# Kernel optimization log

Hardware: AMD Instinct MI355X
Metric: run time of the kernel (lower is better)

Reference implementation:

```python
import jax, jax.numpy as jnp
import numpy as np
from math import pi

FC_IN, FC_OUT = 64, 64
LABEL_NC = 35
B, C, H, W = 2, 64, 128, 128
EPS = 1e-5
SLOPE = 0.01  # torch leaky_relu default


def _pa(h, w):
    # absolute normalized coordinates, matches init_pos buffers
    xs = (jnp.arange(h, dtype=jnp.float32) / h) * 2.0 - 1.0
    ys = (jnp.arange(w, dtype=jnp.float32) / w) * 2.0 - 1.0
    px = jnp.broadcast_to(xs[:, None], (h, w))
    py = jnp.broadcast_to(ys[None, :], (h, w))
    return jnp.stack([px, py], 0)  # (2,h,w)


def _coords(h, w):
    # f0=3; while-loop runs once (f=3 -> f=1), so exactly 4 channels
    f = 3.0
    ang_x = 2.0 * pi * jnp.remainder(jnp.arange(w, dtype=jnp.float32), f) / f
    ang_y = 2.0 * pi * jnp.remainder(jnp.arange(h, dtype=jnp.float32), f) / f
    xcos = jnp.broadcast_to(jnp.cos(ang_x)[None, :], (h, w))
    xsin = jnp.broadcast_to(jnp.sin(ang_x)[None, :], (h, w))
    ycos = jnp.broadcast_to(jnp.cos(ang_y)[:, None], (h, w))
    ysin = jnp.broadcast_to(jnp.sin(ang_y)[:, None], (h, w))
    return jnp.stack([xcos, xsin, ycos, ysin], 0)  # (4,h,w)


def _nearest(t, h, w):
    # F.interpolate(mode='nearest') index map: floor(i*in/out)
    ih = jnp.arange(h) * t.shape[2] // h
    iw = jnp.arange(w) * t.shape[3] // w
    return t[:, :, ih][:, :, :, iw]


def setup_inputs() -> dict:
    key = jax.random.key(0)
    ks = jax.random.split(key, 7)
    return {
        "x": jax.random.normal(ks[0], (B, C, H, W), jnp.float32),
        "layout": jax.random.normal(ks[1], (B, LABEL_NC, H, W), jnp.float32),
        "pr": jax.random.normal(ks[2], (B, 2, H, W), jnp.float32),
        "conv_w": jax.random.normal(ks[3], (1, 10), jnp.float32) * 0.02,
        "conv_b": jnp.zeros((1,), jnp.float32),
        "W_table": jax.random.normal(ks[4], (LABEL_NC, FC_IN * FC_OUT), jnp.float32),
        "b_table": jax.random.normal(ks[5], (LABEL_NC, FC_OUT), jnp.float32) * 0.02,
        "pl": jax.random.normal(ks[6], (2, H, W), jnp.float32),
    }


def reference(x, layout, pr, conv_w, conv_b, W_table, b_table, pl):
    b, c, h, w = x.shape
    pa = jnp.broadcast_to(_pa(h, w)[None], (b, 2, h, w))
    plb = jnp.broadcast_to(pl[None], (b, 2, h, w))
    coords = jnp.broadcast_to(_coords(h, w)[None], (b, 4, h, w))
    prr = _nearest(pr, h, w)
    pos = jnp.concatenate([pa, plb, prr, coords], axis=1)  # (B,10,h,w)
    # 1x1 conv to a single channel, broadcast-added over C
    x = x + jnp.einsum('bchw,oc->bohw', pos, conv_w) + conv_b[None, :, None, None]
    # argmax-routed per-pixel affine params
    lay = _nearest(layout, h, w)
    arg = jnp.argmax(lay, axis=1)  # (B,h,w) int
    Wg = W_table[arg].reshape(b, h, w, FC_IN, FC_OUT)  # huge gathered tensor (as in original)
    bg = b_table[arg]  # (B,h,w,FC_OUT)
    xh = jnp.transpose(x, (0, 2, 3, 1))  # (B,h,w,C)
    y = jnp.einsum('bhwc,bhwco->bhwo', xh, Wg) + bg
    y = jnp.transpose(y, (0, 3, 1, 2))  # (B,FC_OUT,h,w)
    # instance norm (no affine, biased variance, eps=1e-5)
    mu = jnp.mean(y, axis=(2, 3), keepdims=True)
    var = jnp.var(y, axis=(2, 3), keepdims=True)
    y = (y - mu) * jax.lax.rsqrt(var + EPS)
    return jnp.where(y >= 0, y, SLOPE * y)
```

## Files before the change

kernel.cpp:

```cpp
#include <hip/hip_runtime.h>

#define HH 128
#define WW 128
#define NPIX (HH*WW)
#define NC 35
#define NB1 512
#define NCHK 16
#define CAP (NCHK*64)
#define NGB (NC*NCHK)
#define NG (2*NGB)

__global__ __launch_bounds__(256) void prep_kernel(
    const float* __restrict__ x, const float* __restrict__ layout,
    const float* __restrict__ pr, const float* __restrict__ cw,
    const float* __restrict__ cb, const float* __restrict__ pl,
    float* __restrict__ xt, int* __restrict__ argbuf, int* __restrict__ hist)
{
    __shared__ float s_t[64*65];
    __shared__ float s_s[64];
    __shared__ int   s_hist[NC];

    const int t  = threadIdx.x;
    const int bk = blockIdx.x;
    const int b  = bk >> 8;
    const int p0 = (bk & 255) << 6;
    const int h  = p0 >> 7;
    const int w0 = p0 & 127;

    if (t < NC) s_hist[t] = 0;

    const float4* x4 = (const float4*)x + (size_t)b*64*4096 + (p0 >> 2);
    #pragma unroll
    for (int k = 0; k < 4; ++k) {
        int f = k*256 + t;
        int c = f >> 4, i = f & 15;
        float4 q = x4[c*4096 + i];
        int base = c*65 + i*4;
        s_t[base+0]=q.x; s_t[base+1]=q.y; s_t[base+2]=q.z; s_t[base+3]=q.w;
    }

    int bi = -1;
    if (t < 64) {
        int w = w0 + t;
        float pxv = (float)h * (2.0f/128.0f) - 1.0f;
        float pyv = (float)w * (2.0f/128.0f) - 1.0f;
        float pl0 = pl[h*WW + w];
        float pl1 = pl[NPIX + h*WW + w];
        float pr0 = pr[((b*2+0)*HH + h)*WW + w];
        float pr1 = pr[((b*2+1)*HH + h)*WW + w];
        int kx = w % 3, kyy = h % 3;
        const float C1 = -0.5f, S1 = 0.86602540378443864676f;
        float xcv = (kx==0)  ? 1.0f : C1;
        float xsv = (kx==0)  ? 0.0f : ((kx==1)  ? S1 : -S1);
        float ycv = (kyy==0) ? 1.0f : C1;
        float ysv = (kyy==0) ? 0.0f : ((kyy==1) ? S1 : -S1);
        s_s[t] = cb[0] + pxv*cw[0] + pyv*cw[1] + pl0*cw[2] + pl1*cw[3]
               + pr0*cw[4] + pr1*cw[5] + xcv*cw[6] + xsv*cw[7]
               + ycv*cw[8] + ysv*cw[9];
    } else if (t < 128) {
        int lane = t - 64;
        const float* lp = layout + (size_t)(b*NC)*NPIX + p0 + lane;
        float best = lp[0]; int bj = 0;
        #pragma unroll
        for (int c = 1; c < NC; ++c) {
            float v = lp[(size_t)c*NPIX];
            if (v > best) { best = v; bj = c; }
        }
        bi = bj;
        argbuf[b*NPIX + p0 + lane] = bj;
    }
    __syncthreads();

    if (bi >= 0) atomicAdd(&s_hist[bi], 1);

    float4* xt4 = (float4*)xt + ((size_t)b*NPIX + p0)*16;
    #pragma unroll
    for (int k = 0; k < 4; ++k) {
        int g = k*256 + t;
        int p = g >> 4, c4 = g & 15;
        float sp = s_s[p];
        float4 q;
        q.x = s_t[(c4*4+0)*65 + p] + sp;
        q.y = s_t[(c4*4+1)*65 + p] + sp;
        q.z = s_t[(c4*4+2)*65 + p] + sp;
        q.w = s_t[(c4*4+3)*65 + p] + sp;
        xt4[p*16 + c4] = q;
    }
    __syncthreads();
    if (t < NC) hist[t*NB1 + bk] = s_hist[t];
}

__global__ __launch_bounds__(256) void scan_kernel(
    const int* __restrict__ hist, int* __restrict__ boff, int* __restrict__ cnt)
{
    __shared__ int s[256];
    const int e = blockIdx.x;
    const int b = e / NC, l = e % NC;
    const int t = threadIdx.x;
    int v = hist[l*NB1 + b*256 + t];
    s[t] = v;
    __syncthreads();
    #pragma unroll
    for (int off = 1; off < 256; off <<= 1) {
        int nv = (t >= off) ? s[t-off] : 0;
        __syncthreads();
        s[t] += nv;
        __syncthreads();
    }
    boff[l*NB1 + b*256 + t] = s[t] - v;
    if (t == 255) cnt[e] = s[255];
}

__global__ __launch_bounds__(64) void scatter_kernel(
    const int* __restrict__ argbuf, const int* __restrict__ boff,
    int* __restrict__ list)
{
    __shared__ int s_loc[NC];
    const int t  = threadIdx.x;
    const int bk = blockIdx.x;
    const int b  = bk >> 8;
    const int p0 = (bk & 255) << 6;
    if (t < NC) s_loc[t] = 0;
    __syncthreads();
    int l = argbuf[b*NPIX + p0 + t];
    int r = atomicAdd(&s_loc[l], 1);
    int pos = boff[l*NB1 + bk] + r;
    list[(b*NC + l)*CAP + pos] = p0 + t;
}

__global__ __launch_bounds__(256) void gemm_kernel(
    const float* __restrict__ Wt, const float* __restrict__ bt,
    const float* __restrict__ xt, const int* __restrict__ cnt,
    const int* __restrict__ list, float* __restrict__ yt,
    float* __restrict__ psum, float* __restrict__ pss)
{
    const int g     = blockIdx.x;
    const int bl    = g >> 4;
    const int chunk = g & (NCHK-1);
    const int t = threadIdx.x, wv = t >> 6, lane = t & 63;
    const int n = cnt[bl];
    const int base = chunk * 64;
    if (base >= n) {
        if (wv == 0) { psum[lane*NG + g] = 0.f; pss[lane*NG + g] = 0.f; }
        return;
    }
    const int m = min(64, n - base);
    const int b = bl / NC, l = bl % NC;

    __shared__ float s_x[64*64];
    __shared__ int   s_pix[64];
    __shared__ float s_red[4][64][2];

    if (t < 64) s_pix[t] = (t < m) ? list[bl*CAP + base + t] : 0;
    __syncthreads();

    {
        int p = t >> 2, j = t & 3;
        if (p < m) {
            const float4* r = (const float4*)xt + ((size_t)b*NPIX + s_pix[p])*16;
            #pragma unroll
            for (int k = 0; k < 4; ++k)
                ((float4*)(s_x + p*64 + j*16))[k] = r[j*4 + k];
        }
    }

    float Wcol[64];
    const float* Wl = Wt + l*4096 + lane;
    #pragma unroll
    for (int c = 0; c < 64; ++c) Wcol[c] = Wl[c*64];
    float bias = bt[l*64 + lane];
    __syncthreads();

    float ssum = 0.f, sss = 0.f;
    for (int i = 0; i < 16; ++i) {
        int p = wv*16 + i;
        if (p < m) {
            float acc = bias;
            const float4* xr = (const float4*)(s_x + p*64);
            #pragma unroll
            for (int c4 = 0; c4 < 16; ++c4) {
                float4 xq = xr[c4];
                acc = fmaf(xq.x, Wcol[4*c4+0], acc);
                acc = fmaf(xq.y, Wcol[4*c4+1], acc);
                acc = fmaf(xq.z, Wcol[4*c4+2], acc);
                acc = fmaf(xq.w, Wcol[4*c4+3], acc);
            }
            yt[((size_t)b*NPIX + s_pix[p])*64 + lane] = acc;
            ssum += acc; sss += acc*acc;
        }
    }
    s_red[wv][lane][0] = ssum;
    s_red[wv][lane][1] = sss;
    __syncthreads();
    if (wv == 0) {
        float S  = s_red[0][lane][0]+s_red[1][lane][0]+s_red[2][lane][0]+s_red[3][lane][0];
        float SS = s_red[0][lane][1]+s_red[1][lane][1]+s_red[2][lane][1]+s_red[3][lane][1];
        psum[lane*NG + g] = S;
        pss [lane*NG + g] = SS;
    }
}

__global__ __launch_bounds__(256) void stats_kernel(
    const float* __restrict__ psum, const float* __restrict__ pss,
    float* __restrict__ stats)
{
    __shared__ float red[256][2];
    const int e = blockIdx.x;
    const int b = e >> 6, o = e & 63;
    const int t = threadIdx.x;
    float S = 0.f, SS = 0.f;
    for (int gl = t; gl < NGB; gl += 256) {
        int g = b*NGB + gl;
        S  += psum[o*NG + g];
        SS += pss [o*NG + g];
    }
    red[t][0] = S; red[t][1] = SS;
    __syncthreads();
    #pragma unroll
    for (int s = 128; s > 0; s >>= 1) {
        if (t < s) { red[t][0] += red[t+s][0]; red[t][1] += red[t+s][1]; }
        __syncthreads();
    }
    if (t == 0) {
        const float invN = 1.0f/16384.0f;
        float mean = red[0][0] * invN;
        float var  = red[0][1] * invN - mean*mean;
        stats[e*2+0] = mean;
        stats[e*2+1] = rsqrtf(var + 1e-5f);
    }
}

__global__ __launch_bounds__(256) void norm_kernel(
    const float* __restrict__ yt, const float* __restrict__ stats,
    float* __restrict__ out)
{
    __shared__ float s_t[64*65];
    __shared__ float s_mean[64], s_rstd[64];

    const int t  = threadIdx.x;
    const int bk = blockIdx.x;
    const int b  = bk >> 8;
    const int p0 = (bk & 255) << 6;

    if (t < 64) {
        s_mean[t] = stats[(b*64+t)*2+0];
        s_rstd[t] = stats[(b*64+t)*2+1];
    }

    const float4* y4 = (const float4*)yt + ((size_t)b*NPIX + p0)*16;
    #pragma unroll
    for (int k = 0; k < 4; ++k) {
        int g = k*256 + t;
        int p = g >> 4, o4 = g & 15;
        float4 q = y4[p*16 + o4];
        int base = (o4*4)*65 + p;
        s_t[base]     = q.x;
        s_t[base+65]  = q.y;
        s_t[base+130] = q.z;
        s_t[base+195] = q.w;
    }
    __syncthreads();

    const int p = t & 63, og = (t >> 6) * 16;
    float* op = out + ((size_t)b*64 + og)*NPIX + p0 + p;
    #pragma unroll
    for (int kk = 0; kk < 16; ++kk) {
        int o = og + kk;
        float v = (s_t[o*65 + p] - s_mean[o]) * s_rstd[o];
        op[(size_t)kk*NPIX] = (v >= 0.f) ? v : 0.01f*v;
    }
}

extern "C" void kernel_launch(void* const* d_in, const int* in_sizes, int n_in,
                              void* d_out, int out_size, void* d_ws, size_t ws_size,
                              hipStream_t stream) {
    const float* x      = (const float*)d_in[0];
    const float* layout = (const float*)d_in[1];
    const float* pr     = (const float*)d_in[2];
    const float* cw     = (const float*)d_in[3];
    const float* cb     = (const float*)d_in[4];
    const float* Wt     = (const float*)d_in[5];
    const float* bt     = (const float*)d_in[6];
    const float* pl     = (const float*)d_in[7];
    float* out = (float*)d_out;

    char* ws = (char*)d_ws;
    size_t off = 0;
    float* xt     = (float*)(ws + off); off += (size_t)2*NPIX*64*4;
    float* yt     = (float*)(ws + off); off += (size_t)2*NPIX*64*4;
    int*   argbuf = (int*)  (ws + off); off += (size_t)2*NPIX*4;
    int*   hist   = (int*)  (ws + off); off += (size_t)NC*NB1*4;
    int*   boff   = (int*)  (ws + off); off += (size_t)NC*NB1*4;
    int*   cnt    = (int*)  (ws + off); off += 512;
    int*   list   = (int*)  (ws + off); off += (size_t)2*NC*CAP*4;
    float* psum   = (float*)(ws + off); off += (size_t)64*NG*4;
    float* pss    = (float*)(ws + off); off += (size_t)64*NG*4;
    float* stats  = (float*)(ws + off); off += 128*2*4;

    prep_kernel   <<<NB1, 256, 0, stream>>>(x, layout, pr, cw, cb, pl, xt, argbuf, hist);
    scan_kernel   <<<2*NC, 256, 0, stream>>>(hist, boff, cnt);
    scatter_kernel<<<NB1,  64, 0, stream>>>(argbuf, boff, list);
    gemm_kernel   <<<NG,  256, 0, stream>>>(Wt, bt, xt, cnt, list, yt, psum, pss);
    stats_kernel  <<<128, 256, 0, stream>>>(psum, pss, stats);
    norm_kernel   <<<NB1, 256, 0, stream>>>(yt, stats, out);
}
```

Measured before the change: 109.5 us.

## Replace histogram/scan/scatter bucketing with in-block ballot compaction per window

Removes the histogram, prefix-scan and scatter kernels. Each gemm block now scans a 1024-pixel window of the argmax buffer for its label, building a compact pixel list in shared memory with wave ballots and then looping over 64-pixel tiles. This cuts two launches and the global list traffic. In exchange, every block rereads its window of argbuf, many blocks will find few or no matches, and load balance depends on label distribution per window. It also splits the dot product into four accumulators and transposes the partial-sum layout for coalesced writes.

```diff
diff --git a/kernel.cpp b/kernel.cpp
--- a/kernel.cpp
+++ b/kernel.cpp
@@ -5,20 +5,18 @@
 #define NPIX (HH*WW)
 #define NC 35
 #define NB1 512
-#define NCHK 16
-#define CAP (NCHK*64)
-#define NGB (NC*NCHK)
+#define NWIN 16
+#define NGB (NC*NWIN)
 #define NG (2*NGB)
 
 __global__ __launch_bounds__(256) void prep_kernel(
     const float* __restrict__ x, const float* __restrict__ layout,
     const float* __restrict__ pr, const float* __restrict__ cw,
     const float* __restrict__ cb, const float* __restrict__ pl,
-    float* __restrict__ xt, int* __restrict__ argbuf, int* __restrict__ hist)
+    float* __restrict__ xt, int* __restrict__ argbuf)
 {
     __shared__ float s_t[64*65];
     __shared__ float s_s[64];
-    __shared__ int   s_hist[NC];
 
     const int t  = threadIdx.x;
     const int bk = blockIdx.x;
@@ -27,8 +25,6 @@
     const int h  = p0 >> 7;
     const int w0 = p0 & 127;
 
-    if (t < NC) s_hist[t] = 0;
-
     const float4* x4 = (const float4*)x + (size_t)b*64*4096 + (p0 >> 2);
     #pragma unroll
     for (int k = 0; k < 4; ++k) {
@@ -39,7 +35,6 @@
         s_t[base+0]=q.x; s_t[base+1]=q.y; s_t[base+2]=q.z; s_t[base+3]=q.w;
     }
 
-    int bi = -1;
     if (t < 64) {
         int w = w0 + t;
         float pxv = (float)h * (2.0f/128.0f) - 1.0f;
@@ -66,12 +61,9 @@
             float v = lp[(size_t)c*NPIX];
             if (v > best) { best = v; bj = c; }
         }
-        bi = bj;
         argbuf[b*NPIX + p0 + lane] = bj;
     }
     __syncthreads();
-
-    if (bi >= 0) atomicAdd(&s_hist[bi], 1);
 
     float4* xt4 = (float4*)xt + ((size_t)b*NPIX + p0)*16;
     #pragma unroll
@@ -86,81 +78,44 @@
         q.w = s_t[(c4*4+3)*65 + p] + sp;
         xt4[p*16 + c4] = q;
     }
-    __syncthreads();
-    if (t < NC) hist[t*NB1 + bk] = s_hist[t];
-}
-
-__global__ __launch_bounds__(256) void scan_kernel(
-    const int* __restrict__ hist, int* __restrict__ boff, int* __restrict__ cnt)
-{
-    __shared__ int s[256];
-    const int e = blockIdx.x;
-    const int b = e / NC, l = e % NC;
-    const int t = threadIdx.x;
-    int v = hist[l*NB1 + b*256 + t];
-    s[t] = v;
-    __syncthreads();
-    #pragma unroll
-    for (int off = 1; off < 256; off <<= 1) {
-        int nv = (t >= off) ? s[t-off] : 0;
-        __syncthreads();
-        s[t] += nv;
-        __syncthreads();
-    }
-    boff[l*NB1 + b*256 + t] = s[t] - v;
-    if (t == 255) cnt[e] = s[255];
-}
-
-__global__ __launch_bounds__(64) void scatter_kernel(
-    const int* __restrict__ argbuf, const int* __restrict__ boff,
-    int* __restrict__ list)
-{
-    __shared__ int s_loc[NC];
-    const int t  = threadIdx.x;
-    const int bk = blockIdx.x;
-    const int b  = bk >> 8;
-    const int p0 = (bk & 255) << 6;
-    if (t < NC) s_loc[t] = 0;
-    __syncthreads();
-    int l = argbuf[b*NPIX + p0 + t];
-    int r = atomicAdd(&s_loc[l], 1);
-    int pos = boff[l*NB1 + bk] + r;
-    list[(b*NC + l)*CAP + pos] = p0 + t;
 }
 
 __global__ __launch_bounds__(256) void gemm_kernel(
     const float* __restrict__ Wt, const float* __restrict__ bt,
-    const float* __restrict__ xt, const int* __restrict__ cnt,
-    const int* __restrict__ list, float* __restrict__ yt,
-    float* __restrict__ psum, float* __restrict__ pss)
-{
-    const int g     = blockIdx.x;
-    const int bl    = g >> 4;
-    const int chunk = g & (NCHK-1);
+    const float* __restrict__ xt, const int* __restrict__ argbuf,
+    float* __restrict__ yt, float* __restrict__ psum, float* __restrict__ pss)
+{
+    const int g   = blockIdx.x;
+    const int b   = g / NGB;
+    const int rem = g % NGB;
+    const int l   = rem >> 4;
+    const int win = rem & (NWIN-1);
     const int t = threadIdx.x, wv = t >> 6, lane = t & 63;
-    const int n = cnt[bl];
-    const int base = chunk * 64;
-    if (base >= n) {
-        if (wv == 0) { psum[lane*NG + g] = 0.f; pss[lane*NG + g] = 0.f; }
-        return;
-    }
-    const int m = min(64, n - base);
-    const int b = bl / NC, l = bl % NC;
-
+
+    __shared__ int   s_list[1024];
+    __shared__ int   s_n;
     __shared__ float s_x[64*64];
-    __shared__ int   s_pix[64];
     __shared__ float s_red[4][64][2];
 
-    if (t < 64) s_pix[t] = (t < m) ? list[bl*CAP + base + t] : 0;
-    __syncthreads();
-
-    {
-        int p = t >> 2, j = t & 3;
-        if (p < m) {
-            const float4* r = (const float4*)xt + ((size_t)b*NPIX + s_pix[p])*16;
-            #pragma unroll
-            for (int k = 0; k < 4; ++k)
-                ((float4*)(s_x + p*64 + j*16))[k] = r[j*4 + k];
+    if (t == 0) s_n = 0;
+    __syncthreads();
+
+    const int wpix = win*1024;
+    #pragma unroll
+    for (int j = 0; j < 4; ++j) {
+        int idx = wv*256 + j*64 + lane;
+        int a = argbuf[b*NPIX + wpix + idx];
+        bool match = (a == l);
+        unsigned long long mask = __ballot(match);
+        int total = __popcll(mask);
+        if (total) {
+            int base = 0;
+            if (lane == 0) base = atomicAdd(&s_n, total);
+            base = __shfl(base, 0);
+            if (match) {
+                int rank = __popcll(mask & ((1ull << lane) - 1ull));
+                s_list[base + rank] = wpix + idx;
+            }
         }
     }
 
@@ -170,33 +125,51 @@
     for (int c = 0; c < 64; ++c) Wcol[c] = Wl[c*64];
     float bias = bt[l*64 + lane];
     __syncthreads();
+    const int m = s_n;
 
     float ssum = 0.f, sss = 0.f;
-    for (int i = 0; i < 16; ++i) {
-        int p = wv*16 + i;
-        if (p < m) {
-            float acc = bias;
-            const float4* xr = (const float4*)(s_x + p*64);
+    for (int base0 = 0; base0 < m; base0 += 64) {
+        int mm = min(64, m - base0);
+        {
+            int p = t >> 2, j = t & 3;
+            if (p < mm) {
+                const float4* r = (const float4*)xt + ((size_t)b*NPIX + s_list[base0+p])*16;
+                #pragma unroll
+                for (int k = 0; k < 4; ++k)
+                    ((float4*)(s_x + p*64 + j*16))[k] = r[j*4 + k];
+            }
+        }
+        __syncthreads();
+        for (int i = wv; i < mm; i += 4) {
+            const float4* xr = (const float4*)(s_x + i*64);
+            float a0 = bias, a1 = 0.f, a2 = 0.f, a3 = 0.f;
             #pragma unroll
-            for (int c4 = 0; c4 < 16; ++c4) {
-                float4 xq = xr[c4];
-                acc = fmaf(xq.x, Wcol[4*c4+0], acc);
-                acc = fmaf(xq.y, Wcol[4*c4+1], acc);
-                acc = fmaf(xq.z, Wcol[4*c4+2], acc);
-                acc = fmaf(xq.w, Wcol[4*c4+3], acc);
+            for (int c4 = 0; c4 < 16; c4 += 4) {
+                float4 q0 = xr[c4+0], q1 = xr[c4+1], q2 = xr[c4+2], q3 = xr[c4+3];
+                a0 = fmaf(q0.x, Wcol[4*c4+ 0], a0); a0 = fmaf(q0.y, Wcol[4*c4+ 1], a0);
+                a0 = fmaf(q0.z, Wcol[4*c4+ 2], a0); a0 = fmaf(q0.w, Wcol[4*c4+ 3], a0);
+                a1 = fmaf(q1.x, Wcol[4*c4+ 4], a1); a1 = fmaf(q1.y, Wcol[4*c4+ 5], a1);
+                a1 = fmaf(q1.z, Wcol[4*c4+ 6], a1); a1 = fmaf(q1.w, Wcol[4*c4+ 7], a1);
+                a2 = fmaf(q2.x, Wcol[4*c4+ 8], a2); a2 = fmaf(q2.y, Wcol[4*c4+ 9], a2);
+                a2 = fmaf(q2.z, Wcol[4*c4+10], a2); a2 = fmaf(q2.w, Wcol[4*c4+11], a2);
+                a3 = fmaf(q3.x, Wcol[4*c4+12], a3); a3 = fmaf(q3.y, Wcol[4*c4+13], a3);
+                a3 = fmaf(q3.z, Wcol[4*c4+14], a3); a3 = fmaf(q3.w, Wcol[4*c4+15], a3);
             }
-            yt[((size_t)b*NPIX + s_pix[p])*64 + lane] = acc;
+            float acc = (a0 + a1) + (a2 + a3);
+            yt[((size_t)b*NPIX + s_list[base0+i])*64 + lane] = acc;
             ssum += acc; sss += acc*acc;
         }
-    }
+        __syncthreads();
+    }
+
     s_red[wv][lane][0] = ssum;
     s_red[wv][lane][1] = sss;
     __syncthreads();
     if (wv == 0) {
         float S  = s_red[0][lane][0]+s_red[1][lane][0]+s_red[2][lane][0]+s_red[3][lane][0];
         float SS = s_red[0][lane][1]+s_red[1][lane][1]+s_red[2][lane][1]+s_red[3][lane][1];
-        psum[lane*NG + g] = S;
-        pss [lane*NG + g] = SS;
+        psum[g*64 + lane] = S;
+        pss [g*64 + lane] = SS;
     }
 }
 
@@ -211,8 +184,8 @@
     float S = 0.f, SS = 0.f;
     for (int gl = t; gl < NGB; gl += 256) {
         int g = b*NGB + gl;
-        S  += psum[o*NG + g];
-        SS += pss [o*NG + g];
+        S  += psum[g*64 + o];
+        SS += pss [g*64 + o];
     }
     red[t][0] = S; red[t][1] = SS;
     __syncthreads();
@@ -289,18 +262,12 @@
     float* xt     = (float*)(ws + off); off += (size_t)2*NPIX*64*4;
     float* yt     = (float*)(ws + off); off += (size_t)2*NPIX*64*4;
     int*   argbuf = (int*)  (ws + off); off += (size_t)2*NPIX*4;
-    int*   hist   = (int*)  (ws + off); off += (size_t)NC*NB1*4;
-    int*   boff   = (int*)  (ws + off); off += (size_t)NC*NB1*4;
-    int*   cnt    = (int*)  (ws + off); off += 512;
-    int*   list   = (int*)  (ws + off); off += (size_t)2*NC*CAP*4;
-    float* psum   = (float*)(ws + off); off += (size_t)64*NG*4;
-    float* pss    = (float*)(ws + off); off += (size_t)64*NG*4;
+    float* psum   = (float*)(ws + off); off += (size_t)NG*64*4;
+    float* pss    = (float*)(ws + off); off += (size_t)NG*64*4;
     float* stats  = (float*)(ws + off); off += 128*2*4;
 
-    prep_kernel   <<<NB1, 256, 0, stream>>>(x, layout, pr, cw, cb, pl, xt, argbuf, hist);
-    scan_kernel   <<<2*NC, 256, 0, stream>>>(hist, boff, cnt);
-    scatter_kernel<<<NB1,  64, 0, stream>>>(argbuf, boff, list);
-    gemm_kernel   <<<NG,  256, 0, stream>>>(Wt, bt, xt, cnt, list, yt, psum, pss);
-    stats_kernel  <<<128, 256, 0, stream>>>(psum, pss, stats);
-    norm_kernel   <<<NB1, 256, 0, stream>>>(yt, stats, out);
-}
+    prep_kernel <<<NB1, 256, 0, stream>>>(x, layout, pr, cw, cb, pl, xt, argbuf);
+    gemm_kernel <<<NG,  256, 0, stream>>>(Wt, bt, xt, argbuf, yt, psum, pss);
+    stats_kernel<<<128, 256, 0, stream>>>(psum, pss, stats);
+    norm_kernel <<<NB1, 256, 0, stream>>>(yt, stats, out);
+}
```

Measured after the change: 103.4 us. 1.06x faster.
